# Performance work log

Hardware: AMD Instinct MI355X
Metric: run time of the kernel (lower is better)

## Reference

```python
import jax, jax.numpy as jnp
import numpy as np

N_NODES = 100000
N_FEAT = 512
HIDDEN = 64
N_CLASSES = 40
N_EDGES = 3200000
K = 10
ALPHA = 0.1


def setup_inputs() -> dict:
    key = jax.random.key(0)
    k1, k2, k3, k4 = jax.random.split(key, 4)
    x = jax.random.normal(k1, (N_NODES, N_FEAT), dtype=jnp.float32)
    # Glorot-ish scaled linear weights
    W1 = jax.random.normal(k2, (N_FEAT, HIDDEN), dtype=jnp.float32) / np.sqrt(N_FEAT)
    b1 = jnp.zeros((HIDDEN,), dtype=jnp.float32)
    W2 = jax.random.normal(k3, (HIDDEN, N_CLASSES), dtype=jnp.float32) / np.sqrt(HIDDEN)
    b2 = jnp.zeros((N_CLASSES,), dtype=jnp.float32)
    edge_index = jax.random.randint(k4, (2, N_EDGES), 0, N_NODES, dtype=jnp.int64)
    return {"x": x, "W1": W1, "b1": b1, "W2": W2, "b2": b2, "edge_index": edge_index}


def reference(x, W1, b1, W2, b2, edge_index):
    n = x.shape[0]
    # MLP (dropout is identity in eval mode)
    h = jnp.maximum(x @ W1 + b1, 0.0)
    h = h @ W2 + b2  # [N, C]

    # gcn_norm with self-loops: A_hat = D^{-1/2} (A + I) D^{-1/2}
    loops = jnp.arange(n, dtype=edge_index.dtype)
    row = jnp.concatenate([edge_index[0], loops])  # source (gather)
    col = jnp.concatenate([edge_index[1], loops])  # target (scatter)
    deg = jax.ops.segment_sum(jnp.ones(row.shape, dtype=h.dtype), col, num_segments=n)
    dinv = jnp.where(deg > 0, jax.lax.rsqrt(deg), 0.0)
    norm = dinv[row] * dinv[col]  # [E + N]

    h0 = h

    def step(z, _):
        msg = norm[:, None] * z[row]                      # gather + scale
        agg = jax.ops.segment_sum(msg, col, num_segments=n)  # scatter-add
        z = ALPHA * h0 + (1.0 - ALPHA) * agg
        return z, None

    z, _ = jax.lax.scan(step, h0, None, length=K)
    return jax.nn.log_softmax(z, axis=1)
```

## Files before the change

kernel.cpp:

```cpp
#include <hip/hip_runtime.h>
#include <hip/hip_bf16.h>
#include <hip/hip_fp16.h>

#define N_NODES   100000
#define N_FEAT    512
#define HIDDEN    64
#define N_CLASSES 40
#define KITER     10
#define ALPHA     0.1f
#define ZP        64
#define HPITCH    72

typedef __attribute__((ext_vector_type(8))) short bf16x8;
typedef __attribute__((ext_vector_type(4))) float f32x4;

__device__ __forceinline__ float bf2f(unsigned short u) {
    union { unsigned int i; float f; } c;
    c.i = ((unsigned int)u) << 16;
    return c.f;
}
__device__ __forceinline__ unsigned short f2bf(float f) {
    union { float f; unsigned int u; } c; c.f = f;
    unsigned int r = c.u + 0x7FFFu + ((c.u >> 16) & 1u);
    return (unsigned short)(r >> 16);
}

__global__ void zero_flags_kernel(int* __restrict__ flags) {
    if (threadIdx.x < 2) flags[threadIdx.x] = 0;
}

__global__ void detect_float_kernel(const unsigned short* __restrict__ w1raw,
                                    int* __restrict__ flags) {
    int i = blockIdx.x * blockDim.x + threadIdx.x;
    if (i < 32768) {
        unsigned short u = w1raw[i];
        if ((u & 0x7F80u) == 0x7F80u) atomicAdd(&flags[0], 1);
    }
}

__global__ void detect_edge_kernel(const int* __restrict__ ei, int* __restrict__ flags) {
    int i = blockIdx.x * blockDim.x + threadIdx.x;
    if (i < 2048) {
        if (ei[2 * i + 1] != 0) atomicAdd(&flags[1], 1);
    }
}

__device__ __forceinline__ int edge_row(const int* ei, int e, int E, int i64f) {
    return i64f ? ei[2 * e] : ei[e];
}
__device__ __forceinline__ int edge_col(const int* ei, int e, int E, int i64f) {
    return i64f ? ei[2 * E + 2 * e] : ei[E + e];
}

__global__ void pack_w1_kernel(const void* __restrict__ W1p, const int* __restrict__ flags,
                               unsigned short* __restrict__ pb) {
    int idx = blockIdx.x * 256 + threadIdx.x;
    int j    = idx & 7;
    int lane = (idx >> 3) & 63;
    int ktnt = idx >> 9;
    int kt = ktnt & 15, nt = ktnt >> 4;
    int k = kt * 32 + (lane >> 4) * 8 + j;
    int n = nt * 16 + (lane & 15);
    unsigned short v;
    if (flags[0] > 0) v = f2bf(((const float*)W1p)[k * HIDDEN + n]);
    else              v = ((const unsigned short*)W1p)[k * HIDDEN + n];
    pb[idx] = v;
}

__global__ void pack_w2_kernel(const void* __restrict__ W2p, const int* __restrict__ flags,
                               unsigned short* __restrict__ pb2) {
    int idx = blockIdx.x * 256 + threadIdx.x;
    if (idx >= 3072) return;
    int j    = idx & 7;
    int lane = (idx >> 3) & 63;
    int ktnt = idx >> 9;
    int kt = ktnt & 1, nt = ktnt >> 1;
    int k = kt * 32 + (lane >> 4) * 8 + j;
    int n = nt * 16 + (lane & 15);
    unsigned short v = 0;
    if (n < N_CLASSES) {
        if (flags[0] > 0) v = f2bf(((const float*)W2p)[k * N_CLASSES + n]);
        else              v = ((const unsigned short*)W2p)[k * N_CLASSES + n];
    }
    pb2[idx] = v;
}

__global__ __launch_bounds__(256) void mlp_kernel(
    const void* __restrict__ xp,
    const unsigned short* __restrict__ pb,
    const unsigned short* __restrict__ pb2,
    const void* __restrict__ b1p,
    const void* __restrict__ b2p,
    const int* __restrict__ flags,
    float* __restrict__ h0,
    __half* __restrict__ zh0)
{
    __shared__ unsigned short hsb[16 * HPITCH];
    const int t    = threadIdx.x;
    const int wave = t >> 6;
    const int lane = t & 63;
    const int quad = lane >> 4;
    const int ml   = lane & 15;
    const int base = blockIdx.x * 16;
    const int isf32 = flags[0] > 0;

    const bf16x8* pbv = (const bf16x8*)pb;

    f32x4 acc = {0.f, 0.f, 0.f, 0.f};
    if (!isf32) {
        const unsigned short* xrow = (const unsigned short*)xp
                                   + (size_t)(base + ml) * N_FEAT + quad * 8;
        #pragma unroll
        for (int kt = 0; kt < 16; ++kt) {
            bf16x8 a = *(const bf16x8*)(xrow + kt * 32);
            bf16x8 b = pbv[(wave * 16 + kt) * 64 + lane];
            acc = __builtin_amdgcn_mfma_f32_16x16x32_bf16(a, b, acc, 0, 0, 0);
        }
    } else {
        const float* xf = (const float*)xp + (size_t)(base + ml) * N_FEAT + quad * 8;
        #pragma unroll
        for (int kt = 0; kt < 16; ++kt) {
            float4 lo = *(const float4*)(xf + kt * 32);
            float4 hi = *(const float4*)(xf + kt * 32 + 4);
            bf16x8 a;
            a[0] = (short)f2bf(lo.x); a[1] = (short)f2bf(lo.y);
            a[2] = (short)f2bf(lo.z); a[3] = (short)f2bf(lo.w);
            a[4] = (short)f2bf(hi.x); a[5] = (short)f2bf(hi.y);
            a[6] = (short)f2bf(hi.z); a[7] = (short)f2bf(hi.w);
            bf16x8 b = pbv[(wave * 16 + kt) * 64 + lane];
            acc = __builtin_amdgcn_mfma_f32_16x16x32_bf16(a, b, acc, 0, 0, 0);
        }
    }

    float b1v = isf32 ? ((const float*)b1p)[wave * 16 + ml]
                      : bf2f(((const unsigned short*)b1p)[wave * 16 + ml]);
    #pragma unroll
    for (int r = 0; r < 4; ++r)
        hsb[(quad * 4 + r) * HPITCH + wave * 16 + ml] = f2bf(fmaxf(acc[r] + b1v, 0.0f));
    __syncthreads();

    if (wave < 3) {
        const bf16x8* pb2v = (const bf16x8*)pb2;
        f32x4 acc2 = {0.f, 0.f, 0.f, 0.f};
        #pragma unroll
        for (int kt = 0; kt < 2; ++kt) {
            bf16x8 a = *(const bf16x8*)(hsb + ml * HPITCH + kt * 32 + quad * 8);
            bf16x8 b = pb2v[(wave * 2 + kt) * 64 + lane];
            acc2 = __builtin_amdgcn_mfma_f32_16x16x32_bf16(a, b, acc2, 0, 0, 0);
        }
        int n = wave * 16 + ml;
        if (n < N_CLASSES) {
            float b2v = isf32 ? ((const float*)b2p)[n] : bf2f(((const unsigned short*)b2p)[n]);
            #pragma unroll
            for (int r = 0; r < 4; ++r) {
                int node = base + quad * 4 + r;
                float v = acc2[r] + b2v;
                h0[(size_t)node * N_CLASSES + n] = v;
                zh0[(size_t)node * ZP + n] = __float2half(v);
            }
        }
    }
}

__global__ void zero_cnt_kernel(int* __restrict__ cnt) {
    int i = blockIdx.x * blockDim.x + threadIdx.x;
    if (i < N_NODES) cnt[i] = 0;
}

__global__ void count_kernel(const int* __restrict__ ei, const int* __restrict__ flags,
                             int* __restrict__ cnt, int E) {
    int e = blockIdx.x * blockDim.x + threadIdx.x;
    int i64f = flags[1] == 0;
    if (e < E) atomicAdd(&cnt[edge_col(ei, e, E, i64f)], 1);
}

__global__ void dinv_kernel(const int* __restrict__ cnt, float* __restrict__ dinv) {
    int i = blockIdx.x * blockDim.x + threadIdx.x;
    if (i < N_NODES) dinv[i] = rsqrtf((float)cnt[i] + 1.0f);
}

__global__ __launch_bounds__(1024) void scan_kernel(
    const int* __restrict__ cnt, int* __restrict__ rptr, int* __restrict__ wpos, int E)
{
    __shared__ int wsum[16];
    __shared__ int carry_s, tiletot_s;
    const int t = threadIdx.x, wave = t >> 6, lane = t & 63;
    if (t == 0) carry_s = 0;
    __syncthreads();
    for (int base = 0; base < N_NODES; base += 4096) {
        int i0 = base + t * 4;
        int v0 = (i0 + 0 < N_NODES) ? cnt[i0 + 0] : 0;
        int v1 = (i0 + 1 < N_NODES) ? cnt[i0 + 1] : 0;
        int v2 = (i0 + 2 < N_NODES) ? cnt[i0 + 2] : 0;
        int v3 = (i0 + 3 < N_NODES) ? cnt[i0 + 3] : 0;
        int tl = v0 + v1 + v2 + v3;
        int sc = tl;
        #pragma unroll
        for (int off = 1; off < 64; off <<= 1) {
            int u = __shfl_up(sc, off, 64);
            if (lane >= off) sc += u;
        }
        if (lane == 63) wsum[wave] = sc;
        int wexcl = sc - tl;
        __syncthreads();
        if (wave == 0) {
            int wv = (lane < 16) ? wsum[lane] : 0;
            int ws = wv;
            #pragma unroll
            for (int off = 1; off < 16; off <<= 1) {
                int u = __shfl_up(ws, off, 64);
                if (lane >= off) ws += u;
            }
            if (lane < 16) wsum[lane] = ws - wv;
            if (lane == 15) tiletot_s = ws;
        }
        __syncthreads();
        int P  = carry_s + wsum[wave] + wexcl;
        int e0 = P, e1 = P + v0, e2 = e1 + v1, e3 = e2 + v2;
        if (i0 + 0 < N_NODES) { rptr[i0 + 0] = e0; wpos[i0 + 0] = e0; }
        if (i0 + 1 < N_NODES) { rptr[i0 + 1] = e1; wpos[i0 + 1] = e1; }
        if (i0 + 2 < N_NODES) { rptr[i0 + 2] = e2; wpos[i0 + 2] = e2; }
        if (i0 + 3 < N_NODES) { rptr[i0 + 3] = e3; wpos[i0 + 3] = e3; }
        __syncthreads();
        if (t == 0) carry_s += tiletot_s;
        __syncthreads();
    }
    if (t == 0) rptr[N_NODES] = E;
}

__global__ void fill_kernel(const int* __restrict__ ei, const int* __restrict__ flags,
                            const float* __restrict__ dinv, int* __restrict__ wpos,
                            int2* __restrict__ srn, int E)
{
    int e = blockIdx.x * blockDim.x + threadIdx.x;
    int i64f = flags[1] == 0;
    if (e < E) {
        int r = edge_row(ei, e, E, i64f);
        int c = edge_col(ei, e, E, i64f);
        int pos = atomicAdd(&wpos[c], 1);
        srn[pos] = make_int2(r, __float_as_int(dinv[r] * dinv[c]));
    }
}

__global__ __launch_bounds__(256) void prop_kernel(
    const __half* __restrict__ zh, const float* __restrict__ h0,
    const float* __restrict__ dinv, const int* __restrict__ rptr,
    const int2* __restrict__ srn, __half* __restrict__ zout, int E)
{
    const int wave = threadIdx.x >> 6;
    const int lane = threadIdx.x & 63;
    const int g    = lane >> 4;
    const int l    = lane & 15;
    const int node = blockIdx.x * 16 + wave * 4 + g;
    const int c0   = l * 4;

    const int beg = rptr[node];
    const int end = rptr[node + 1];
    int nch = (end - beg + 15) >> 4;
    int m1    = max(nch, __shfl_xor(nch, 16, 64));
    int maxch = max(m1,  __shfl_xor(m1, 32, 64));

    float di = dinv[node];
    uint2 zzs = *(const uint2*)(zh + ((size_t)node << 6) + c0);
    float h00 = 0.f, h01 = 0.f, h02 = 0.f, h03 = 0.f;
    if (c0 < N_CLASSES) {
        const float* hp = h0 + (size_t)node * N_CLASSES + c0;
        h00 = hp[0]; h01 = hp[1]; h02 = hp[2]; h03 = hp[3];
    }

    float a0 = 0.f, a1 = 0.f, a2 = 0.f, a3 = 0.f;
    float b0 = 0.f, b1 = 0.f, b2 = 0.f, b3 = 0.f;

    for (int ch = 0; ch < maxch; ++ch) {
        int idx  = beg + ch * 16 + l;
        bool v   = idx < end;
        int cidx = v ? idx : beg;
        cidx = min(cidx, E - 1);
        int2 ew  = srn[cidx];
        int   sw = ew.x;
        float nw = v ? __int_as_float(ew.y) : 0.0f;

        #pragma unroll
        for (int i = 0; i < 16; i += 2) {
            int   s0 = __shfl(sw, (g << 4) + i,     64);
            float n0 = __shfl(nw, (g << 4) + i,     64);
            int   s1 = __shfl(sw, (g << 4) + i + 1, 64);
            float n1 = __shfl(nw, (g << 4) + i + 1, 64);
            uint2 z0 = *(const uint2*)(zh + ((size_t)s0 << 6) + c0);
            uint2 z1 = *(const uint2*)(zh + ((size_t)s1 << 6) + c0);
            const __half2* p0 = (const __half2*)&z0;
            const __half2* p1 = (const __half2*)&z1;
            float2 f00 = __half22float2(p0[0]);
            float2 f01 = __half22float2(p0[1]);
            float2 f10 = __half22float2(p1[0]);
            float2 f11 = __half22float2(p1[1]);
            a0 = fmaf(n0, f00.x, a0); a1 = fmaf(n0, f00.y, a1);
            a2 = fmaf(n0, f01.x, a2); a3 = fmaf(n0, f01.y, a3);
            b0 = fmaf(n1, f10.x, b0); b1 = fmaf(n1, f10.y, b1);
            b2 = fmaf(n1, f11.x, b2); b3 = fmaf(n1, f11.y, b3);
        }
    }

    if (c0 < N_CLASSES) {
        const __half2* ps = (const __half2*)&zzs;
        float2 s01 = __half22float2(ps[0]);
        float2 s23 = __half22float2(ps[1]);
        float dd = di * di;
        float o0 = ALPHA * h00 + (1.0f - ALPHA) * (a0 + b0 + dd * s01.x);
        float o1 = ALPHA * h01 + (1.0f - ALPHA) * (a1 + b1 + dd * s01.y);
        float o2 = ALPHA * h02 + (1.0f - ALPHA) * (a2 + b2 + dd * s23.x);
        float o3 = ALPHA * h03 + (1.0f - ALPHA) * (a3 + b3 + dd * s23.y);
        __half2 q01 = __floats2half2_rn(o0, o1);
        __half2 q23 = __floats2half2_rn(o2, o3);
        uint2 st;
        st.x = *(unsigned int*)&q01;
        st.y = *(unsigned int*)&q23;
        *(uint2*)(zout + ((size_t)node << 6) + c0) = st;
    }
}

__global__ __launch_bounds__(256) void lsm_kernel(
    const __half* __restrict__ zh, const int* __restrict__ flags, void* __restrict__ outp)
{
    const int wave = threadIdx.x >> 6;
    const int lane = threadIdx.x & 63;
    const int node = blockIdx.x * 4 + wave;
    const int isf32 = flags[0] > 0;

    float v = (lane < N_CLASSES) ? __half2float(zh[(size_t)node * ZP + lane]) : -1e30f;
    float m = v;
    #pragma unroll
    for (int o = 32; o; o >>= 1) m = fmaxf(m, __shfl_xor(m, o, 64));
    float e = (lane < N_CLASSES) ? expf(v - m) : 0.0f;
    float s = e;
    #pragma unroll
    for (int o = 32; o; o >>= 1) s += __shfl_xor(s, o, 64);
    float ls = logf(s);
    if (lane < N_CLASSES) {
        float r = v - m - ls;
        size_t idx = (size_t)node * N_CLASSES + lane;
        if (isf32) ((float*)outp)[idx] = r;
        else       ((__hip_bfloat16*)outp)[idx] = __float2bfloat16(r);
    }
}

extern "C" void kernel_launch(void* const* d_in, const int* in_sizes, int n_in,
                              void* d_out, int out_size, void* d_ws, size_t ws_size,
                              hipStream_t stream)
{
    const void* x  = d_in[0];
    const void* W1 = d_in[1];
    const void* b1 = d_in[2];
    const void* W2 = d_in[3];
    const void* b2 = d_in[4];
    const int* ei = (const int*)d_in[5];
    const int E = in_sizes[5] / 2;

    char* ws = (char*)d_ws;
    size_t off = 0;
    auto carve = [&](size_t bytes) -> void* {
        void* p = ws + off;
        off = (off + bytes + 255) & ~(size_t)255;
        return p;
    };
    float*  h0    = (float*) carve((size_t)N_NODES * N_CLASSES * 4);
    __half* zhA   = (__half*)carve((size_t)N_NODES * ZP * 2);
    __half* zhB   = (__half*)carve((size_t)N_NODES * ZP * 2);
    int*    cnt   = (int*)   carve((size_t)N_NODES * 4);
    float*  dinv  = (float*) carve((size_t)N_NODES * 4);
    int*    rptr  = (int*)   carve((size_t)(N_NODES + 1) * 4);
    int*    wpos  = (int*)   carve((size_t)N_NODES * 4);
    int2*   srn   = (int2*)  carve((size_t)E * 8);
    unsigned short* pb  = (unsigned short*)carve(32768 * 2);
    unsigned short* pb2 = (unsigned short*)carve(3072 * 2);
    int*    flags = (int*)   carve(2 * sizeof(int));
    (void)ws_size; (void)n_in; (void)out_size;

    const int nodeBlocks = N_NODES / 4;
    const int mlpBlocks  = N_NODES / 16;
    const int propBlocks = N_NODES / 16;
    const int nThreads1  = (N_NODES + 255) / 256;
    const int eBlocks    = (E + 255) / 256;

    zero_flags_kernel<<<1, 64, 0, stream>>>(flags);
    detect_float_kernel<<<128, 256, 0, stream>>>((const unsigned short*)W1, flags);
    detect_edge_kernel<<<8, 256, 0, stream>>>(ei, flags);
    pack_w1_kernel<<<128, 256, 0, stream>>>(W1, flags, pb);
    pack_w2_kernel<<<12, 256, 0, stream>>>(W2, flags, pb2);

    mlp_kernel<<<mlpBlocks, 256, 0, stream>>>(x, pb, pb2, b1, b2, flags, h0, zhA);

    zero_cnt_kernel<<<nThreads1, 256, 0, stream>>>(cnt);
    count_kernel<<<eBlocks, 256, 0, stream>>>(ei, flags, cnt, E);
    dinv_kernel<<<nThreads1, 256, 0, stream>>>(cnt, dinv);
    scan_kernel<<<1, 1024, 0, stream>>>(cnt, rptr, wpos, E);
    fill_kernel<<<eBlocks, 256, 0, stream>>>(ei, flags, dinv, wpos, srn, E);

    const __half* zin = zhA;
    __half* zout = zhB;
    const __half* zlast = zhA;
    for (int it = 0; it < KITER; ++it) {
        prop_kernel<<<propBlocks, 256, 0, stream>>>(zin, h0, dinv, rptr, srn, zout, E);
        zlast = zout;
        zin = zout;
        zout = (zout == zhB) ? zhA : zhB;
    }

    lsm_kernel<<<nodeBlocks, 256, 0, stream>>>(zlast, flags, d_out);
}
```

Baseline: 1.270 ms.

## Pre-scale features by dinv, split classes into 16-wide chunks, drop per-edge norm

Propagation now stores u = dinv*z, so each edge contributes an unweighted sum and the per-edge norm array goes away; CSR edges shrink from int2 to a single int source index. Features are laid out as three class chunks of 16 halves (32 bytes per node), and each propagation step runs three launches, one per chunk, so the gathered working set per pass is smaller and more cache-friendly. Nontemporal loads and stores are used for edge indices and outputs, and the MLP now runs after the CSR build so it can apply dinv. The cost is that the edge list is read three times per iteration, there are three times as many launches, and lsm has to divide by dinv, which can amplify fp16 rounding error.

```diff
diff --git a/kernel.cpp b/kernel.cpp
--- a/kernel.cpp
+++ b/kernel.cpp
@@ -8,8 +8,8 @@
 #define N_CLASSES 40
 #define KITER     10
 #define ALPHA     0.1f
-#define ZP        64
 #define HPITCH    72
+#define CSTRIDE   ((size_t)N_NODES * 16)
 
 typedef __attribute__((ext_vector_type(8))) short bf16x8;
 typedef __attribute__((ext_vector_type(4))) float f32x4;
@@ -92,8 +92,9 @@
     const void* __restrict__ b1p,
     const void* __restrict__ b2p,
     const int* __restrict__ flags,
+    const float* __restrict__ dinv,
     float* __restrict__ h0,
-    __half* __restrict__ zh0)
+    __half* __restrict__ u0)
 {
     __shared__ unsigned short hsb[16 * HPITCH];
     const int t    = threadIdx.x;
@@ -151,12 +152,14 @@
         int n = wave * 16 + ml;
         if (n < N_CLASSES) {
             float b2v = isf32 ? ((const float*)b2p)[n] : bf2f(((const unsigned short*)b2p)[n]);
+            int cchunk = n >> 4, jj = n & 15;
             #pragma unroll
             for (int r = 0; r < 4; ++r) {
                 int node = base + quad * 4 + r;
                 float v = acc2[r] + b2v;
                 h0[(size_t)node * N_CLASSES + n] = v;
-                zh0[(size_t)node * ZP + n] = __float2half(v);
+                u0[(size_t)cchunk * CSTRIDE + ((size_t)node << 4) + jj]
+                    = __float2half(dinv[node] * v);
             }
         }
     }
@@ -229,8 +232,7 @@
 }
 
 __global__ void fill_kernel(const int* __restrict__ ei, const int* __restrict__ flags,
-                            const float* __restrict__ dinv, int* __restrict__ wpos,
-                            int2* __restrict__ srn, int E)
+                            int* __restrict__ wpos, int* __restrict__ srow, int E)
 {
     int e = blockIdx.x * blockDim.x + threadIdx.x;
     int i64f = flags[1] == 0;
@@ -238,106 +240,102 @@
         int r = edge_row(ei, e, E, i64f);
         int c = edge_col(ei, e, E, i64f);
         int pos = atomicAdd(&wpos[c], 1);
-        srn[pos] = make_int2(r, __float_as_int(dinv[r] * dinv[c]));
+        __builtin_nontemporal_store(r, &srow[pos]);
     }
 }
 
 __global__ __launch_bounds__(256) void prop_kernel(
-    const __half* __restrict__ zh, const float* __restrict__ h0,
+    const __half* __restrict__ uin, const float* __restrict__ h0,
     const float* __restrict__ dinv, const int* __restrict__ rptr,
-    const int2* __restrict__ srn, __half* __restrict__ zout, int E)
-{
-    const int wave = threadIdx.x >> 6;
-    const int lane = threadIdx.x & 63;
-    const int g    = lane >> 4;
-    const int l    = lane & 15;
-    const int node = blockIdx.x * 16 + wave * 4 + g;
-    const int c0   = l * 4;
-
-    const int beg = rptr[node];
-    const int end = rptr[node + 1];
-    int nch = (end - beg + 15) >> 4;
-    int m1    = max(nch, __shfl_xor(nch, 16, 64));
-    int maxch = max(m1,  __shfl_xor(m1, 32, 64));
-
-    float di = dinv[node];
-    uint2 zzs = *(const uint2*)(zh + ((size_t)node << 6) + c0);
-    float h00 = 0.f, h01 = 0.f, h02 = 0.f, h03 = 0.f;
-    if (c0 < N_CLASSES) {
-        const float* hp = h0 + (size_t)node * N_CLASSES + c0;
-        h00 = hp[0]; h01 = hp[1]; h02 = hp[2]; h03 = hp[3];
-    }
+    const int* __restrict__ srow, __half* __restrict__ uout, int chunk)
+{
+    const int t = threadIdx.x;
+    const int wave = t >> 6;
+    const int lane = t & 63;
+    const int g = lane >> 2, q = lane & 3;
+    const int node = blockIdx.x * 64 + wave * 16 + g;
+    const bool nv = node < N_NODES;
+    const int cls0 = chunk * 16 + (q << 2);
+    const bool cvalid = cls0 < N_CLASSES;
+
+    const __half* ub = uin + (size_t)chunk * CSTRIDE;
+    int beg = 0, end = 0;
+    float di = 0.f;
+    if (nv) { beg = rptr[node]; end = rptr[node + 1]; di = dinv[node]; }
+
+    uint2 su = make_uint2(0u, 0u);
+    if (nv && cvalid) su = *(const uint2*)(ub + ((size_t)node << 4) + (q << 2));
+    float4 h0v = make_float4(0.f, 0.f, 0.f, 0.f);
+    if (nv && cvalid) h0v = *(const float4*)(h0 + (size_t)node * N_CLASSES + cls0);
+
+    int m = (end - beg + 3) >> 2;
+    m = max(m, __shfl_xor(m, 4, 64));
+    m = max(m, __shfl_xor(m, 8, 64));
+    m = max(m, __shfl_xor(m, 16, 64));
+    m = max(m, __shfl_xor(m, 32, 64));
 
     float a0 = 0.f, a1 = 0.f, a2 = 0.f, a3 = 0.f;
-    float b0 = 0.f, b1 = 0.f, b2 = 0.f, b3 = 0.f;
-
-    for (int ch = 0; ch < maxch; ++ch) {
-        int idx  = beg + ch * 16 + l;
-        bool v   = idx < end;
-        int cidx = v ? idx : beg;
-        cidx = min(cidx, E - 1);
-        int2 ew  = srn[cidx];
-        int   sw = ew.x;
-        float nw = v ? __int_as_float(ew.y) : 0.0f;
-
+    for (int ch = 0; ch < m; ++ch) {
+        int idx = beg + (ch << 2) + q;
+        int r = 0;
+        if (idx < end) r = __builtin_nontemporal_load(srow + idx);
         #pragma unroll
-        for (int i = 0; i < 16; i += 2) {
-            int   s0 = __shfl(sw, (g << 4) + i,     64);
-            float n0 = __shfl(nw, (g << 4) + i,     64);
-            int   s1 = __shfl(sw, (g << 4) + i + 1, 64);
-            float n1 = __shfl(nw, (g << 4) + i + 1, 64);
-            uint2 z0 = *(const uint2*)(zh + ((size_t)s0 << 6) + c0);
-            uint2 z1 = *(const uint2*)(zh + ((size_t)s1 << 6) + c0);
-            const __half2* p0 = (const __half2*)&z0;
-            const __half2* p1 = (const __half2*)&z1;
-            float2 f00 = __half22float2(p0[0]);
-            float2 f01 = __half22float2(p0[1]);
-            float2 f10 = __half22float2(p1[0]);
-            float2 f11 = __half22float2(p1[1]);
-            a0 = fmaf(n0, f00.x, a0); a1 = fmaf(n0, f00.y, a1);
-            a2 = fmaf(n0, f01.x, a2); a3 = fmaf(n0, f01.y, a3);
-            b0 = fmaf(n1, f10.x, b0); b1 = fmaf(n1, f10.y, b1);
-            b2 = fmaf(n1, f11.x, b2); b3 = fmaf(n1, f11.y, b3);
-        }
-    }
-
-    if (c0 < N_CLASSES) {
-        const __half2* ps = (const __half2*)&zzs;
-        float2 s01 = __half22float2(ps[0]);
-        float2 s23 = __half22float2(ps[1]);
-        float dd = di * di;
-        float o0 = ALPHA * h00 + (1.0f - ALPHA) * (a0 + b0 + dd * s01.x);
-        float o1 = ALPHA * h01 + (1.0f - ALPHA) * (a1 + b1 + dd * s01.y);
-        float o2 = ALPHA * h02 + (1.0f - ALPHA) * (a2 + b2 + dd * s23.x);
-        float o3 = ALPHA * h03 + (1.0f - ALPHA) * (a3 + b3 + dd * s23.y);
-        __half2 q01 = __floats2half2_rn(o0, o1);
-        __half2 q23 = __floats2half2_rn(o2, o3);
-        uint2 st;
-        st.x = *(unsigned int*)&q01;
-        st.y = *(unsigned int*)&q23;
-        *(uint2*)(zout + ((size_t)node << 6) + c0) = st;
+        for (int j = 0; j < 4; ++j) {
+            int rj = __shfl(r, (g << 2) + j, 64);
+            if (cvalid && (beg + (ch << 2) + j < end)) {
+                uint2 zz = *(const uint2*)(ub + ((size_t)rj << 4) + (q << 2));
+                __half2* ph = (__half2*)&zz;
+                float2 f0 = __half22float2(ph[0]);
+                float2 f1 = __half22float2(ph[1]);
+                a0 += f0.x; a1 += f0.y; a2 += f1.x; a3 += f1.y;
+            }
+        }
+    }
+
+    if (nv && cvalid) {
+        __half2* ps = (__half2*)&su;
+        float2 s0 = __half22float2(ps[0]);
+        float2 s1 = __half22float2(ps[1]);
+        float o0 = ALPHA * h0v.x + (1.0f - ALPHA) * di * (a0 + s0.x);
+        float o1 = ALPHA * h0v.y + (1.0f - ALPHA) * di * (a1 + s0.y);
+        float o2 = ALPHA * h0v.z + (1.0f - ALPHA) * di * (a2 + s1.x);
+        float o3 = ALPHA * h0v.w + (1.0f - ALPHA) * di * (a3 + s1.y);
+        __half2 q01 = __floats2half2_rn(di * o0, di * o1);
+        __half2 q23 = __floats2half2_rn(di * o2, di * o3);
+        unsigned int lo = *(unsigned int*)&q01;
+        unsigned int hi = *(unsigned int*)&q23;
+        unsigned long long pk = ((unsigned long long)hi << 32) | (unsigned long long)lo;
+        __builtin_nontemporal_store(pk,
+            (unsigned long long*)(uout + (size_t)chunk * CSTRIDE + ((size_t)node << 4) + (q << 2)));
     }
 }
 
 __global__ __launch_bounds__(256) void lsm_kernel(
-    const __half* __restrict__ zh, const int* __restrict__ flags, void* __restrict__ outp)
+    const __half* __restrict__ u, const float* __restrict__ dinv,
+    const int* __restrict__ flags, void* __restrict__ outp)
 {
     const int wave = threadIdx.x >> 6;
     const int lane = threadIdx.x & 63;
     const int node = blockIdx.x * 4 + wave;
     const int isf32 = flags[0] > 0;
 
-    float v = (lane < N_CLASSES) ? __half2float(zh[(size_t)node * ZP + lane]) : -1e30f;
-    float m = v;
+    float di = dinv[node];
+    float v = -1e30f;
+    if (lane < N_CLASSES) {
+        int cchunk = lane >> 4, j = lane & 15;
+        __half uu = u[(size_t)cchunk * CSTRIDE + ((size_t)node << 4) + j];
+        v = __half2float(uu) / di;
+    }
+    float mx = v;
     #pragma unroll
-    for (int o = 32; o; o >>= 1) m = fmaxf(m, __shfl_xor(m, o, 64));
-    float e = (lane < N_CLASSES) ? expf(v - m) : 0.0f;
+    for (int o = 32; o; o >>= 1) mx = fmaxf(mx, __shfl_xor(mx, o, 64));
+    float e = (lane < N_CLASSES) ? expf(v - mx) : 0.0f;
     float s = e;
     #pragma unroll
     for (int o = 32; o; o >>= 1) s += __shfl_xor(s, o, 64);
     float ls = logf(s);
     if (lane < N_CLASSES) {
-        float r = v - m - ls;
+        float r = v - mx - ls;
         size_t idx = (size_t)node * N_CLASSES + lane;
         if (isf32) ((float*)outp)[idx] = r;
         else       ((__hip_bfloat16*)outp)[idx] = __float2bfloat16(r);
@@ -364,21 +362,20 @@
         return p;
     };
     float*  h0    = (float*) carve((size_t)N_NODES * N_CLASSES * 4);
-    __half* zhA   = (__half*)carve((size_t)N_NODES * ZP * 2);
-    __half* zhB   = (__half*)carve((size_t)N_NODES * ZP * 2);
+    __half* uA    = (__half*)carve(3 * CSTRIDE * 2);
+    __half* uB    = (__half*)carve(3 * CSTRIDE * 2);
     int*    cnt   = (int*)   carve((size_t)N_NODES * 4);
     float*  dinv  = (float*) carve((size_t)N_NODES * 4);
     int*    rptr  = (int*)   carve((size_t)(N_NODES + 1) * 4);
     int*    wpos  = (int*)   carve((size_t)N_NODES * 4);
-    int2*   srn   = (int2*)  carve((size_t)E * 8);
+    int*    srow  = (int*)   carve((size_t)E * 4);
     unsigned short* pb  = (unsigned short*)carve(32768 * 2);
     unsigned short* pb2 = (unsigned short*)carve(3072 * 2);
     int*    flags = (int*)   carve(2 * sizeof(int));
     (void)ws_size; (void)n_in; (void)out_size;
 
-    const int nodeBlocks = N_NODES / 4;
     const int mlpBlocks  = N_NODES / 16;
-    const int propBlocks = N_NODES / 16;
+    const int propBlocks = (N_NODES + 63) / 64;
     const int nThreads1  = (N_NODES + 255) / 256;
     const int eBlocks    = (E + 255) / 256;
 
@@ -388,23 +385,24 @@
     pack_w1_kernel<<<128, 256, 0, stream>>>(W1, flags, pb);
     pack_w2_kernel<<<12, 256, 0, stream>>>(W2, flags, pb2);
 
-    mlp_kernel<<<mlpBlocks, 256, 0, stream>>>(x, pb, pb2, b1, b2, flags, h0, zhA);
-
     zero_cnt_kernel<<<nThreads1, 256, 0, stream>>>(cnt);
     count_kernel<<<eBlocks, 256, 0, stream>>>(ei, flags, cnt, E);
     dinv_kernel<<<nThreads1, 256, 0, stream>>>(cnt, dinv);
     scan_kernel<<<1, 1024, 0, stream>>>(cnt, rptr, wpos, E);
-    fill_kernel<<<eBlocks, 256, 0, stream>>>(ei, flags, dinv, wpos, srn, E);
-
-    const __half* zin = zhA;
-    __half* zout = zhB;
-    const __half* zlast = zhA;
+    fill_kernel<<<eBlocks, 256, 0, stream>>>(ei, flags, wpos, srow, E);
+
+    mlp_kernel<<<mlpBlocks, 256, 0, stream>>>(x, pb, pb2, b1, b2, flags, dinv, h0, uA);
+
+    const __half* zin = uA;
+    __half* zout = uB;
+    const __half* zlast = uA;
     for (int it = 0; it < KITER; ++it) {
-        prop_kernel<<<propBlocks, 256, 0, stream>>>(zin, h0, dinv, rptr, srn, zout, E);
+        for (int c = 0; c < 3; ++c)
+            prop_kernel<<<propBlocks, 256, 0, stream>>>(zin, h0, dinv, rptr, srow, zout, c);
         zlast = zout;
         zin = zout;
-        zout = (zout == zhB) ? zhA : zhB;
-    }
-
-    lsm_kernel<<<nodeBlocks, 256, 0, stream>>>(zlast, flags, d_out);
-}
+        zout = (zout == uB) ? uA : uB;
+    }
+
+    lsm_kernel<<<N_NODES / 4, 256, 0, stream>>>(zlast, dinv, flags, d_out);
+}
```

After: 2.075 ms. 63.4% more time.
